# Kernel optimization log

Hardware: AMD Instinct MI355X
Metric: run time of the kernel (lower is better)

The kernel has to match this reference:

```python
import jax, jax.numpy as jnp
import numpy as np

SCALE = 0.08838834764831845  # 1/sqrt(128)
SOFT_CAP = 0.0               # module default soft_cap=0 -> disabled


def setup_inputs() -> dict:
    key = jax.random.key(0)
    k1, k2, k3, k4, k5 = jax.random.split(key, 5)
    R, B, Hq, Hk, Dq, Dv = 4, 16, 32, 8, 128, 128
    P, PAGE, M = 8192, 1, 2048  # pages per rank, page_size, max pages per seq
    q = jax.random.normal(k1, (B, Hq, Dq), dtype=jnp.float16)
    k_cache = jax.random.normal(k2, (R, P, PAGE, Hk, Dq), dtype=jnp.float16)
    v_cache = jax.random.normal(k3, (R, P, PAGE, Hk, Dv), dtype=jnp.float16)
    # at least 1 valid token per rank per sequence
    global_kv_lens = jax.random.randint(k4, (R, B), 1, M * PAGE + 1, dtype=jnp.int32)
    block_table = jax.random.randint(k5, (R, B, M), 0, P, dtype=jnp.int32)
    return {"q": q, "k_cache": k_cache, "v_cache": v_cache,
            "global_kv_lens": global_kv_lens, "block_table": block_table}


def _flash_decode(q, k_cache, v_cache, global_kv_lens, block_table):
    R, P, PAGE, Hk, Dq = k_cache.shape
    B, Hq, _ = q.shape
    G = Hq // Hk                      # GQA group size
    M = block_table.shape[-1]
    K = M * PAGE                      # max kv tokens per rank per seq
    Dv = v_cache.shape[-1]

    # paged gather per rank: kc[bt] -> [B, M, PAGE, Hk, D]
    kg = jax.vmap(lambda kc, bt: kc[bt])(k_cache, block_table)
    vg = jax.vmap(lambda vc, bt: vc[bt])(v_cache, block_table)
    kg = kg.reshape(R, B, K, Hk, Dq).astype(jnp.float32)
    vg = vg.reshape(R, B, K, Hk, Dv).astype(jnp.float32)

    qf = q.astype(jnp.float32).reshape(B, Hk, G, Dq)
    # scores [R, B, Hk, G, K]
    s = jnp.einsum('bhgd,rbkhd->rbhgk', qf, kg) * SCALE
    if SOFT_CAP > 0:
        s = SOFT_CAP * jnp.tanh(s / SOFT_CAP)

    valid = jnp.arange(K)[None, None, :] < global_kv_lens[:, :, None]  # [R,B,K]
    s = jnp.where(valid[:, :, None, None, :], s, -jnp.inf)

    # per-rank partial softmax stats (what gqa_local_kernels_fused produces)
    m = jnp.max(s, axis=-1)                      # [R,B,Hk,G]
    p = jnp.exp(s - m[..., None])
    l = jnp.sum(p, axis=-1)                      # [R,B,Hk,G]
    o = jnp.einsum('rbhgk,rbkhd->rbhgd', p, vg)  # [R,B,Hk,G,Dv]

    # cross-rank lse-weighted reduce (gqa_global_reduce_fused)
    m_g = jnp.max(m, axis=0)                     # [B,Hk,G]
    w = jnp.exp(m - m_g[None])                   # [R,B,Hk,G]
    o_tot = jnp.sum(w[..., None] * o, axis=0)    # [B,Hk,G,Dv]
    l_tot = jnp.sum(w * l, axis=0)               # [B,Hk,G]
    out = (o_tot / l_tot[..., None]).reshape(B, Hq, Dv)
    return out.astype(jnp.float32)


def reference(q, k_cache, v_cache, global_kv_lens, block_table):
    return _flash_decode(q, k_cache, v_cache, global_kv_lens, block_table)
```

## Files before the change

### kernel.cpp

```cpp
#include <hip/hip_runtime.h>
#include <math.h>


typedef float f32x4 __attribute__((ext_vector_type(4)));

#define R_ 4
#define B_ 16
#define HQ_ 32
#define HK_ 8
#define G_ 4
#define D_ 128
#define P_ 8192
#define M_ 2048
#define HKD (HK_ * D_)
#define NS 8
#define T_ 4
#define DP 3
#define WV 2
#define SC2 (0.08838834764831845f * 1.4426950408889634f)
#define MNEG (-1.0e30f)

__device__ __forceinline__ int clampP(int p) {
  return p < 0 ? 0 : (p >= P_ ? P_ - 1 : p);
}

__global__ __launch_bounds__(WV * 64) void fd_partial(
    const float* __restrict__ q, const float* __restrict__ kc,
    const float* __restrict__ vc, const int* __restrict__ lens,
    const int* __restrict__ bt, float* __restrict__ ws_m,
    float* __restrict__ ws_l, float* __restrict__ ws_o) {
  __shared__ unsigned s_pg[WV][256];
  __shared__ float s_k[WV][DP][T_ * D_];
  __shared__ float s_v[WV][DP][T_ * D_];

  const int lane = threadIdx.x & 63;
  const int w = threadIdx.x >> 6;
  const int gw = blockIdx.x * WV + w;
  const int s = gw & (NS - 1);
  const int hk = (gw >> 3) & (HK_ - 1);
  const int b = (gw >> 6) & (B_ - 1);
  const int r = gw >> 10;

  const int tg = lane >> 4;
  const int dl = lane & 15;

  int kvlen = lens[r * B_ + b];
  kvlen = kvlen < 0 ? 0 : (kvlen > M_ ? M_ : kvlen);
  const int chunk = (((kvlen + NS - 1) / NS) + T_ - 1) & ~(T_ - 1);
  const int t0 = s * chunk;
  int t1 = t0 + chunk;
  if (t1 > kvlen) t1 = kvlen;
  const int ct = t1 - t0;
  if (ct <= 0) {
    if (lane == 0) {
#pragma unroll
      for (int h = 0; h < G_; ++h) ws_m[gw * G_ + h] = MNEG;
    }
    return;
  }
  const int cm1 = ct - 1;
  const int nT = (ct + T_ - 1) >> 2;

  float qf[G_][8];
  {
    const float* qp = q + ((size_t)b * HQ_ + hk * G_) * D_;
#pragma unroll
    for (int h = 0; h < G_; ++h) {
      f32x4 a = *(const f32x4*)(qp + h * D_ + dl * 4);
      f32x4 c = *(const f32x4*)(qp + h * D_ + 64 + dl * 4);
#pragma unroll
      for (int j = 0; j < 4; ++j) {
        qf[h][j] = a[j] * SC2;
        qf[h][4 + j] = c[j] * SC2;
      }
    }
  }

  {
    const int* btrow = bt + (r * B_ + b) * M_ + t0;
#pragma unroll
    for (int t = 0; t < 256; t += 64) {
      const int idx = t + lane;
      const int tt = idx > cm1 ? cm1 : idx;
      s_pg[w][idx] = ((unsigned)clampP(btrow[tt])) << 12;
    }
  }

  const char* kb = (const char*)kc + ((size_t)r * P_) * 4096 + hk * 512;
  const char* vb = (const char*)vc + ((size_t)r * P_) * 4096 + hk * 512;
  const unsigned* pgw = s_pg[w];
  const unsigned lo16 = ((unsigned)(lane & 31)) << 4;

  float m[G_], l[G_], acc[G_][8];
#pragma unroll
  for (int h = 0; h < G_; ++h) {
    m[h] = MNEG;
    l[h] = 0.f;
#pragma unroll
    for (int j = 0; j < 8; ++j) acc[h][j] = 0.f;
  }

  asm volatile("s_waitcnt vmcnt(0) lgkmcnt(0)" ::: "memory");

  auto stage = [&](int k, int sl) {
#pragma unroll
    for (int j = 0; j < 2; ++j) {
      int tau = T_ * k + 2 * j + (lane >> 5);
      tau = tau > cm1 ? cm1 : tau;
      const unsigned pgo = pgw[tau];
      __builtin_amdgcn_global_load_lds((const float*)(kb + pgo + lo16),
                                       &s_k[w][sl][j * 256], 16, 0, 0);
      __builtin_amdgcn_global_load_lds((const float*)(vb + pgo + lo16),
                                       &s_v[w][sl][j * 256], 16, 0, 0);
    }
  };

  stage(0, 0);
  stage(1, 1);
  stage(2, 2);

  int sl = 0;
  for (int i = 0; i < nT; ++i) {
    asm volatile("s_waitcnt vmcnt(8)" ::: "memory");
    __builtin_amdgcn_sched_barrier(0);

    const float* kp = &s_k[w][sl][tg * D_];
    const float* vp = &s_v[w][sl][tg * D_];
    float kr[8], vr[8];
    {
      f32x4 a = *(const f32x4*)(kp + dl * 4);
      f32x4 c = *(const f32x4*)(kp + 64 + dl * 4);
#pragma unroll
      for (int j = 0; j < 4; ++j) { kr[j] = a[j]; kr[4 + j] = c[j]; }
    }
    float d0 = 0.f, d1 = 0.f, d2 = 0.f, d3 = 0.f;
#pragma unroll
    for (int j = 0; j < 8; ++j) {
      d0 += qf[0][j] * kr[j];
      d1 += qf[1][j] * kr[j];
      d2 += qf[2][j] * kr[j];
      d3 += qf[3][j] * kr[j];
    }
#pragma unroll
    for (int msk = 1; msk <= 8; msk <<= 1) {
      d0 += __shfl_xor(d0, msk);
      d1 += __shfl_xor(d1, msk);
      d2 += __shfl_xor(d2, msk);
      d3 += __shfl_xor(d3, msk);
    }
    {
      f32x4 a = *(const f32x4*)(vp + dl * 4);
      f32x4 c = *(const f32x4*)(vp + 64 + dl * 4);
#pragma unroll
      for (int j = 0; j < 4; ++j) { vr[j] = a[j]; vr[4 + j] = c[j]; }
    }
    const bool valid = (T_ * i + tg) < ct;
    float sH[G_];
    sH[0] = valid ? d0 : -INFINITY;
    sH[1] = valid ? d1 : -INFINITY;
    sH[2] = valid ? d2 : -INFINITY;
    sH[3] = valid ? d3 : -INFINITY;
#pragma unroll
    for (int h = 0; h < G_; ++h) {
      if (sH[h] > m[h]) {
        const float rs = exp2f(m[h] - sH[h]);
        l[h] *= rs;
#pragma unroll
        for (int j = 0; j < 8; ++j) acc[h][j] *= rs;
        m[h] = sH[h];
      }
      const float p = exp2f(sH[h] - m[h]);
      l[h] += p;
#pragma unroll
      for (int j = 0; j < 8; ++j) acc[h][j] += p * vr[j];
    }

    __builtin_amdgcn_sched_barrier(0);
    stage(i + DP, sl);
    sl = (sl == DP - 1) ? 0 : sl + 1;
  }
  asm volatile("s_waitcnt vmcnt(0)" ::: "memory");

#pragma unroll
  for (int h = 0; h < G_; ++h) {
#pragma unroll
    for (int off = 16; off <= 32; off <<= 1) {
      const float mo = __shfl_xor(m[h], off);
      const float lo = __shfl_xor(l[h], off);
      float ao[8];
#pragma unroll
      for (int j = 0; j < 8; ++j) ao[j] = __shfl_xor(acc[h][j], off);
      const float mn = fmaxf(m[h], mo);
      const float se = exp2f(m[h] - mn);
      const float so_ = exp2f(mo - mn);
      l[h] = l[h] * se + lo * so_;
#pragma unroll
      for (int j = 0; j < 8; ++j) acc[h][j] = acc[h][j] * se + ao[j] * so_;
      m[h] = mn;
    }
  }

  if (tg == 0) {
#pragma unroll
    for (int h = 0; h < G_; ++h) {
      float* wp = ws_o + ((size_t)gw * G_ + h) * D_;
      f32x4 a, c;
#pragma unroll
      for (int j = 0; j < 4; ++j) { a[j] = acc[h][j]; c[j] = acc[h][4 + j]; }
      *(f32x4*)(wp + dl * 4) = a;
      *(f32x4*)(wp + 64 + dl * 4) = c;
    }
  }
  if (lane == 0) {
#pragma unroll
    for (int h = 0; h < G_; ++h) {
      ws_m[gw * G_ + h] = m[h];
      ws_l[gw * G_ + h] = l[h];
    }
  }
}

__global__ __launch_bounds__(128) void fd_reduce(
    const float* __restrict__ ws_m, const float* __restrict__ ws_l,
    const float* __restrict__ ws_o, float* __restrict__ out) {
  const int row = blockIdx.x;
  const int g = row % G_;
  const int hk = (row / G_) % HK_;
  const int b = row / (G_ * HK_);
  const int d = threadIdx.x;

  float mf = MNEG;
  for (int r = 0; r < R_; ++r)
    for (int s2 = 0; s2 < NS; ++s2) {
      int rec = ((r * B_ + b) * HK_ + hk) * NS + s2;
      mf = fmaxf(mf, ws_m[rec * G_ + g]);
    }
  float of = 0.f, lf = 0.f;
  for (int r = 0; r < R_; ++r)
    for (int s2 = 0; s2 < NS; ++s2) {
      int rec = ((r * B_ + b) * HK_ + hk) * NS + s2;
      float wt = exp2f(ws_m[rec * G_ + g] - mf);
      of += wt * ws_o[(size_t)(rec * G_ + g) * D_ + d];
      lf += wt * ws_l[rec * G_ + g];
    }
  out[(size_t)(b * HQ_ + hk * G_ + g) * D_ + d] = of / lf;
}

typedef float f32x4_ __attribute__((ext_vector_type(4)));
__device__ __forceinline__ void load8u(const float* __restrict__ ubase,
                                       unsigned boff, float o[8]) {
  const f32x4* p = (const f32x4*)((const char*)ubase + boff);
  f32x4 a = p[0];
  f32x4 b = p[1];
#pragma unroll
  for (int j = 0; j < 4; ++j) { o[j] = a[j]; o[4 + j] = b[j]; }
}

__global__ __launch_bounds__(256) void fd_mono(
    const float* __restrict__ q, const float* __restrict__ kc,
    const float* __restrict__ vc, const int* __restrict__ lens,
    const int* __restrict__ bt, float* __restrict__ out) {
  const int hk = blockIdx.x % HK_;
  const int b = blockIdx.x / HK_;
  const int lane = threadIdx.x & 63;
  const int g = threadIdx.x >> 6;
  const int tg = lane >> 4;
  const int ds = (lane & 15) * 8;
  const unsigned dsb = ds * 4u + ((unsigned)hk << 9);

  float qf[8];
  load8u(q + (size_t)(b * HQ_ + hk * G_ + g) * D_ + ds, 0u, qf);
#pragma unroll
  for (int j = 0; j < 8; ++j) qf[j] *= SC2;

  float m = MNEG, l = 0.f, acc[8];
#pragma unroll
  for (int j = 0; j < 8; ++j) acc[j] = 0.f;

  for (int r = 0; r < R_; ++r) {
    int kvlen = lens[r * B_ + b];
    if (kvlen < 0) kvlen = 0;
    if (kvlen > M_) kvlen = M_;
    const int* btrow = bt + (r * B_ + b) * M_;
    const float* kb = kc + (size_t)r * P_ * HKD;
    const float* vb = vc + (size_t)r * P_ * HKD;

#pragma unroll 1
    for (int t = 0; t < kvlen; t += 4) {
      const int ta = t + tg;
      const bool va = ta < kvlen;
      const unsigned oa = ((unsigned)clampP(btrow[va ? ta : 0]) << 12) + dsb;
      float ka[8], wa[8];
      load8u(kb, oa, ka);
      load8u(vb, oa, wa);

      float da = 0.f;
#pragma unroll
      for (int j = 0; j < 8; ++j) da += qf[j] * ka[j];
#pragma unroll
      for (int msk = 1; msk <= 8; msk <<= 1) da += __shfl_xor(da, msk);

      const float sa = va ? da : -INFINITY;
      const float mn = fmaxf(m, sa);
      const float sc = exp2f(m - mn);
      const float pa = exp2f(sa - mn);
      m = mn;
      l = l * sc + pa;
#pragma unroll
      for (int j = 0; j < 8; ++j) acc[j] = acc[j] * sc + pa * wa[j];
    }
  }

#pragma unroll
  for (int off = 16; off <= 32; off <<= 1) {
    const float mo = __shfl_xor(m, off);
    const float lo = __shfl_xor(l, off);
    float ao[8];
#pragma unroll
    for (int j = 0; j < 8; ++j) ao[j] = __shfl_xor(acc[j], off);
    const float mn = fmaxf(m, mo);
    const float se = exp2f(m - mn);
    const float so_ = exp2f(mo - mn);
    l = l * se + lo * so_;
#pragma unroll
    for (int j = 0; j < 8; ++j) acc[j] = acc[j] * se + ao[j] * so_;
    m = mn;
  }

  if (lane < 16) {
    float inv = (l > 0.f) ? 1.0f / l : 0.f;
#pragma unroll
    for (int j = 0; j < 8; ++j)
      out[(size_t)(b * HQ_ + hk * G_ + g) * D_ + ds + j] = acc[j] * inv;
  }
}

extern "C" void kernel_launch(void* const* d_in, const int* in_sizes, int n_in,
                              void* d_out, int out_size, void* d_ws,
                              size_t ws_size, hipStream_t stream) {
  const float* q = (const float*)d_in[0];
  const float* kc = (const float*)d_in[1];
  const float* vc = (const float*)d_in[2];
  const int* lens = (const int*)d_in[3];
  const int* bt = (const int*)d_in[4];
  float* out = (float*)d_out;

  const int nrec = R_ * B_ * HK_ * NS;
  const size_t need =
      (size_t)nrec * (size_t)(2 * G_ + G_ * D_) * sizeof(float);

  if (need <= ws_size) {
    float* ws_m = (float*)d_ws;
    float* ws_l = ws_m + (size_t)nrec * G_;
    float* ws_o = ws_l + (size_t)nrec * G_;
    fd_partial<<<nrec / WV, WV * 64, 0, stream>>>(q, kc, vc, lens, bt, ws_m,
                                                  ws_l, ws_o);
    fd_reduce<<<B_ * HK_ * G_, 128, 0, stream>>>(ws_m, ws_l, ws_o, out);
  } else {
    fd_mono<<<B_ * HK_, 256, 0, stream>>>(q, kc, vc, lens, bt, out);
  }
}
```

Before: 112.4 us.

## Bucket-sort page indices per sequence to improve gather locality

After: 132.3 us. 1.18x slower.

```diff
diff --git a/kernel.cpp b/kernel.cpp
--- a/kernel.cpp
+++ b/kernel.cpp
@@ -13,7 +13,9 @@
 #define P_ 8192
 #define M_ 2048
 #define HKD (HK_ * D_)
-#define NS 8
+#define NR 8
+#define NBK 256
+#define PROW 2112
 #define T_ 4
 #define DP 3
 #define WV 2
@@ -24,10 +26,45 @@
   return p < 0 ? 0 : (p >= P_ ? P_ - 1 : p);
 }
 
+__global__ __launch_bounds__(256) void fd_compact(
+    const int* __restrict__ lens, const int* __restrict__ bt,
+    unsigned* __restrict__ ws_pages) {
+  __shared__ int hist[NBK];
+  __shared__ int cur[NBK];
+  const int rb = blockIdx.x;
+  const int tid = threadIdx.x;
+  int kvlen = lens[rb];
+  kvlen = kvlen < 1 ? 1 : (kvlen > M_ ? M_ : kvlen);
+  const int* btrow = bt + rb * M_;
+
+  for (int i = tid; i < NBK; i += 256) hist[i] = 0;
+  __syncthreads();
+  for (int t = tid; t < kvlen; t += 256)
+    atomicAdd(&hist[clampP(btrow[t]) >> 5], 1);
+  __syncthreads();
+  if (tid == 0) {
+    int pos = 0;
+    for (int j = 0; j < NBK; ++j) {
+      cur[j] = pos;
+      pos += hist[j];
+    }
+  }
+  __syncthreads();
+  unsigned* prow = ws_pages + (size_t)rb * PROW;
+  for (int t = tid; t < kvlen; t += 256) {
+    const int p = clampP(btrow[t]);
+    const int d = atomicAdd(&cur[p >> 5], 1);
+    prow[d] = ((unsigned)p) << 12;
+  }
+  __syncthreads();
+  const unsigned last = prow[kvlen - 1];
+  for (int i = kvlen + tid; i < PROW; i += 256) prow[i] = last;
+}
+
 __global__ __launch_bounds__(WV * 64) void fd_partial(
     const float* __restrict__ q, const float* __restrict__ kc,
     const float* __restrict__ vc, const int* __restrict__ lens,
-    const int* __restrict__ bt, float* __restrict__ ws_m,
+    const unsigned* __restrict__ ws_pages, float* __restrict__ ws_m,
     float* __restrict__ ws_l, float* __restrict__ ws_o) {
   __shared__ unsigned s_pg[WV][256];
   __shared__ float s_k[WV][DP][T_ * D_];
@@ -36,21 +73,21 @@
   const int lane = threadIdx.x & 63;
   const int w = threadIdx.x >> 6;
   const int gw = blockIdx.x * WV + w;
-  const int s = gw & (NS - 1);
-  const int hk = (gw >> 3) & (HK_ - 1);
-  const int b = (gw >> 6) & (B_ - 1);
-  const int r = gw >> 10;
+  const int s = gw >> 9;
+  const int rbh = gw & 511;
+  const int hk = rbh & (HK_ - 1);
+  const int rb = rbh >> 3;
+  const int b = rb & (B_ - 1);
+  const int r = rb >> 4;
 
   const int tg = lane >> 4;
   const int dl = lane & 15;
 
-  int kvlen = lens[r * B_ + b];
-  kvlen = kvlen < 0 ? 0 : (kvlen > M_ ? M_ : kvlen);
-  const int chunk = (((kvlen + NS - 1) / NS) + T_ - 1) & ~(T_ - 1);
-  const int t0 = s * chunk;
-  int t1 = t0 + chunk;
-  if (t1 > kvlen) t1 = kvlen;
-  const int ct = t1 - t0;
+  int kvlen = lens[rb];
+  kvlen = kvlen < 1 ? 1 : (kvlen > M_ ? M_ : kvlen);
+  const int qn = (((kvlen + NR - 1) / NR) + 3) & ~3;
+  const int start = s * qn;
+  int ct = kvlen - start;
   if (ct <= 0) {
     if (lane == 0) {
 #pragma unroll
@@ -58,6 +95,7 @@
     }
     return;
   }
+  if (ct > qn) ct = qn;
   const int cm1 = ct - 1;
   const int nT = (ct + T_ - 1) >> 2;
 
@@ -77,12 +115,12 @@
   }
 
   {
-    const int* btrow = bt + (r * B_ + b) * M_ + t0;
+    const unsigned* plist = ws_pages + (size_t)rb * PROW + start;
 #pragma unroll
     for (int t = 0; t < 256; t += 64) {
       const int idx = t + lane;
       const int tt = idx > cm1 ? cm1 : idx;
-      s_pg[w][idx] = ((unsigned)clampP(btrow[tt])) << 12;
+      s_pg[w][idx] = plist[tt];
     }
   }
 
@@ -231,22 +269,21 @@
 
   float mf = MNEG;
   for (int r = 0; r < R_; ++r)
-    for (int s2 = 0; s2 < NS; ++s2) {
-      int rec = ((r * B_ + b) * HK_ + hk) * NS + s2;
+    for (int s = 0; s < NR; ++s) {
+      const int rec = s * 512 + (r * B_ + b) * HK_ + hk;
       mf = fmaxf(mf, ws_m[rec * G_ + g]);
     }
   float of = 0.f, lf = 0.f;
   for (int r = 0; r < R_; ++r)
-    for (int s2 = 0; s2 < NS; ++s2) {
-      int rec = ((r * B_ + b) * HK_ + hk) * NS + s2;
-      float wt = exp2f(ws_m[rec * G_ + g] - mf);
-      of += wt * ws_o[(size_t)(rec * G_ + g) * D_ + d];
+    for (int s = 0; s < NR; ++s) {
+      const int rec = s * 512 + (r * B_ + b) * HK_ + hk;
+      const float wt = exp2f(ws_m[rec * G_ + g] - mf);
+      of += wt * ws_o[((size_t)rec * G_ + g) * D_ + d];
       lf += wt * ws_l[rec * G_ + g];
     }
   out[(size_t)(b * HQ_ + hk * G_ + g) * D_ + d] = of / lf;
 }
 
-typedef float f32x4_ __attribute__((ext_vector_type(4)));
 __device__ __forceinline__ void load8u(const float* __restrict__ ubase,
                                        unsigned boff, float o[8]) {
   const f32x4* p = (const f32x4*)((const char*)ubase + boff);
@@ -266,7 +303,7 @@
   const int g = threadIdx.x >> 6;
   const int tg = lane >> 4;
   const int ds = (lane & 15) * 8;
-  const unsigned dsb = ds * 4u + ((unsigned)hk << 9);
+  const unsigned dsb = ds * 4u;
 
   float qf[8];
   load8u(q + (size_t)(b * HQ_ + hk * G_ + g) * D_ + ds, 0u, qf);
@@ -282,8 +319,8 @@
     if (kvlen < 0) kvlen = 0;
     if (kvlen > M_) kvlen = M_;
     const int* btrow = bt + (r * B_ + b) * M_;
-    const float* kb = kc + (size_t)r * P_ * HKD;
-    const float* vb = vc + (size_t)r * P_ * HKD;
+    const float* kb = kc + (size_t)r * P_ * HKD + (size_t)hk * D_;
+    const float* vb = vc + (size_t)r * P_ * HKD + (size_t)hk * D_;
 
 #pragma unroll 1
     for (int t = 0; t < kvlen; t += 4) {
@@ -345,16 +382,21 @@
   const int* bt = (const int*)d_in[4];
   float* out = (float*)d_out;
 
-  const int nrec = R_ * B_ * HK_ * NS;
-  const size_t need =
-      (size_t)nrec * (size_t)(2 * G_ + G_ * D_) * sizeof(float);
+  const int nrec = NR * R_ * B_ * HK_;
+  const size_t sz_pages = (size_t)R_ * B_ * PROW * 4;
+  const size_t sz_ml = (size_t)nrec * G_ * 4;
+  const size_t sz_o = (size_t)nrec * G_ * D_ * 4;
+  const size_t need = sz_pages + 2 * sz_ml + sz_o;
 
   if (need <= ws_size) {
-    float* ws_m = (float*)d_ws;
-    float* ws_l = ws_m + (size_t)nrec * G_;
-    float* ws_o = ws_l + (size_t)nrec * G_;
-    fd_partial<<<nrec / WV, WV * 64, 0, stream>>>(q, kc, vc, lens, bt, ws_m,
-                                                  ws_l, ws_o);
+    char* p = (char*)d_ws;
+    unsigned* ws_pages = (unsigned*)p;  p += sz_pages;
+    float* ws_m = (float*)p;            p += sz_ml;
+    float* ws_l = (float*)p;            p += sz_ml;
+    float* ws_o = (float*)p;
+    fd_compact<<<R_ * B_, 256, 0, stream>>>(lens, bt, ws_pages);
+    fd_partial<<<nrec / WV, WV * 64, 0, stream>>>(q, kc, vc, lens, ws_pages,
+                                                  ws_m, ws_l, ws_o);
     fd_reduce<<<B_ * HK_ * G_, 128, 0, stream>>>(ws_m, ws_l, ws_o, out);
   } else {
     fd_mono<<<B_ * HK_, 256, 0, stream>>>(q, kc, vc, lens, bt, out);
```
